# Kernel optimization log

Hardware: AMD Instinct MI355X
Metric: run time of the kernel (lower is better)

## Reference

```python
import jax, jax.numpy as jnp
import numpy as np

N = 50000          # nodes
E = 800000         # edges (avg degree 16)
F = 128            # in_dim = num_hidden*heads = pred_dim
H = 4              # attention heads per layer
D = 32             # num_hidden (per-head dim)
R = 11             # rel_num
L = 2              # num_layers
SCALE = float(1.0 / np.sqrt(D))


def setup_inputs() -> dict:
    key = jax.random.key(0)
    ks = jax.random.split(key, 16)
    inputs = jax.random.normal(ks[0], (N, F), jnp.float32)
    edge_types = jax.random.randint(ks[1], (E,), 0, R)
    src = jax.random.randint(ks[2], (E,), 0, N)
    dst = jax.random.randint(ks[3], (E,), 0, N)
    centrality = jax.random.uniform(ks[4], (N,), jnp.float32)
    rel_emb = jax.random.normal(ks[5], (R, F), jnp.float32) * 0.1
    # stacked per-layer projection weights (both layers have F -> H*D = F)
    Wq = jax.random.normal(ks[6], (L, F, H * D), jnp.float32) * 0.05
    Wk = jax.random.normal(ks[7], (L, F, H * D), jnp.float32) * 0.05
    Wv = jax.random.normal(ks[8], (L, F, H * D), jnp.float32) * 0.05
    We = jax.random.normal(ks[9], (L, F, H * D), jnp.float32) * 0.05
    bq = jnp.zeros((L, H * D), jnp.float32)
    bk = jnp.zeros((L, H * D), jnp.float32)
    bv = jnp.zeros((L, H * D), jnp.float32)
    be = jnp.zeros((L, H * D), jnp.float32)
    W_out = jax.random.normal(ks[10], (H * D, 1), jnp.float32) * 0.05
    b_out = jnp.zeros((1,), jnp.float32)
    gamma = jnp.ones((1,), jnp.float32)
    beta = jnp.zeros((1,), jnp.float32)
    return {"inputs": inputs, "edge_types": edge_types, "src": src, "dst": dst,
            "centrality": centrality, "rel_emb": rel_emb,
            "Wq": Wq, "bq": bq, "Wk": Wk, "bk": bk, "Wv": Wv, "bv": bv,
            "We": We, "be": be, "W_out": W_out, "b_out": b_out,
            "gamma": gamma, "beta": beta}


def _segment_softmax(score, dst, n):
    # score: [E, H]; softmax over incoming edges of each dst node
    m = jax.ops.segment_max(score, dst, num_segments=n)          # [N, H]
    ex = jnp.exp(score - m[dst])                                  # [E, H]
    s = jax.ops.segment_sum(ex, dst, num_segments=n)              # [N, H]
    return ex / (s[dst] + 1e-9)


def reference(inputs, edge_types, src, dst, centrality, rel_emb,
              Wq, bq, Wk, bk, Wv, bv, We, be, W_out, b_out, gamma, beta):
    h = inputs                                   # [N, F]
    ef = rel_emb[edge_types]                     # [E, pred_dim] relational edge embedding
    for l in range(L):
        q = (h @ Wq[l] + bq[l]).reshape(N, H, D)
        k = (h @ Wk[l] + bk[l]).reshape(N, H, D)
        v = (h @ Wv[l] + bv[l]).reshape(N, H, D)
        e = (ef @ We[l] + be[l]).reshape(E, H, D)
        # edge_mode="add": edge features added to keys/values on each edge
        ke = k[src] + e                           # [E, H, D]
        score = jnp.sum(q[dst] * ke, axis=-1) * SCALE   # [E, H]
        attn = _segment_softmax(score, dst, N)          # [E, H]
        msg = attn[:, :, None] * (v[src] + e)           # [E, H, D]
        agg = jax.ops.segment_sum(msg, dst, num_segments=N)  # [N, H, D]
        # identity residual (in_dim == H*D) + ELU activation
        h = jax.nn.elu(agg.reshape(N, H * D) + h)
    logits = h @ W_out + b_out                    # [N, 1]
    logits = jax.nn.relu((centrality * gamma + beta)[:, None] * logits)
    return logits
```

## Files before the change

kernel.cpp:

```cpp
#include <hip/hip_runtime.h>
#include <hip/hip_bf16.h>
#include <math.h>

#define SCALE_C 0.17677669529663687f
#define CAPP 64

typedef short bf16x8 __attribute__((ext_vector_type(8)));
typedef float f32x4 __attribute__((ext_vector_type(4)));


__global__ __launch_bounds__(256) void scatter_pad_k(
    const int* __restrict__ dst, const int* __restrict__ src, const int* __restrict__ etype,
    int E, int* __restrict__ cnt, int* __restrict__ bins) {
  int e = blockIdx.x * 256 + threadIdx.x;
  if (e < E) {
    int d = dst[e];
    int pos = atomicAdd(&cnt[d], 1);
    if (pos < CAPP) bins[(d << 6) + pos] = src[e] | (etype[e] << 20);
  }
}


__global__ __launch_bounds__(256) void prep_k(
    const float* __restrict__ Wq, const float* __restrict__ Wk, const float* __restrict__ Wv,
    __hip_bfloat16* __restrict__ wf,
    const float* __restrict__ rel_emb, const float* __restrict__ We, const float* __restrict__ be,
    float* __restrict__ re, int R, int* __restrict__ cnt, int N, int reb) {
  int b = blockIdx.x;
  if (b < 48) {
    int tid = b * 256 + threadIdx.x;
    int lane = tid & 63;
    int frag = tid >> 6;
    int ks = frag & 3;
    int ct = (frag >> 2) & 7;
    int mat = frag >> 5;
    int l = mat / 3, m = mat % 3;
    const float* W = ((m == 0) ? Wq : (m == 1) ? Wk : Wv) + (size_t)l * 128 * 128;
    int nn = ct * 16 + (lane & 15);
    int k0 = ks * 32 + (lane >> 4) * 8;
    __hip_bfloat16 tmp[8];
    #pragma unroll
    for (int j = 0; j < 8; ++j) tmp[j] = __float2bfloat16(W[(size_t)(k0 + j) * 128 + nn]);
    *(uint4*)&wf[(size_t)frag * 64 * 8 + (size_t)lane * 8] = *(const uint4*)tmp;
  } else if (b < 48 + reb) {
    int idx = (b - 48) * 256 + threadIdx.x;
    int tot = 2 * R * 128;
    if (idx >= tot) return;
    int c = idx & 127;
    int r = (idx >> 7) % R;
    int l = idx / (R * 128);
    const float* W = We + (size_t)l * 128 * 128;
    float acc = be[l * 128 + c];
    for (int kk = 0; kk < 128; ++kk) acc += rel_emb[r * 128 + kk] * W[kk * 128 + c];
    re[idx] = acc;
  } else {
    int idx = (b - 48 - reb) * 256 + threadIdx.x;
    int nq = N >> 2;
    if (idx < nq) ((uint4*)cnt)[idx] = make_uint4(0, 0, 0, 0);
    if (idx == nq) for (int k = nq << 2; k < N; ++k) cnt[k] = 0;
  }
}


__global__ __launch_bounds__(128) void qkv_k(
    const float* __restrict__ X, const __hip_bfloat16* __restrict__ wf,
    const float* __restrict__ bq, const float* __restrict__ bk, const float* __restrict__ bv,
    __hip_bfloat16* __restrict__ qo, __hip_bfloat16* __restrict__ kvo, int n) {
  __shared__ __hip_bfloat16 kvt[2][32][264];
  int wid = threadIdx.x >> 6;
  int lane = threadIdx.x & 63;
  int row0 = blockIdx.x * 64 + wid * 32;
  if (row0 >= n) return;
  int cl = lane & 15;
  int quad = lane >> 4;

  bf16x8 afrag[2][4];
  #pragma unroll
  for (int s = 0; s < 2; ++s) {
    int arow = row0 + s * 16 + cl;
    bool av = arow < n;
    const float* xr = X + (size_t)arow * 128 + quad * 8;
    #pragma unroll
    for (int ks = 0; ks < 4; ++ks) {
      float4 x0 = av ? *(const float4*)(xr + ks * 32)     : make_float4(0.f, 0.f, 0.f, 0.f);
      float4 x1 = av ? *(const float4*)(xr + ks * 32 + 4) : make_float4(0.f, 0.f, 0.f, 0.f);
      union { bf16x8 v; __hip_bfloat16 h[8]; } fu;
      fu.h[0] = __float2bfloat16(x0.x); fu.h[1] = __float2bfloat16(x0.y);
      fu.h[2] = __float2bfloat16(x0.z); fu.h[3] = __float2bfloat16(x0.w);
      fu.h[4] = __float2bfloat16(x1.x); fu.h[5] = __float2bfloat16(x1.y);
      fu.h[6] = __float2bfloat16(x1.z); fu.h[7] = __float2bfloat16(x1.w);
      afrag[s][ks] = fu.v;
    }
  }
  const uint4* wfu = (const uint4*)wf;

  #pragma unroll
  for (int ct = 0; ct < 8; ++ct) {
    f32x4 a0 = {0.f, 0.f, 0.f, 0.f}, a1 = {0.f, 0.f, 0.f, 0.f};
    #pragma unroll
    for (int ks = 0; ks < 4; ++ks) {
      uint4 braw = wfu[((size_t)ct * 4 + ks) * 64 + lane];
      bf16x8 bfr = __builtin_bit_cast(bf16x8, braw);
      a0 = __builtin_amdgcn_mfma_f32_16x16x32_bf16(afrag[0][ks], bfr, a0, 0, 0, 0);
      a1 = __builtin_amdgcn_mfma_f32_16x16x32_bf16(afrag[1][ks], bfr, a1, 0, 0, 0);
    }
    int c = ct * 16 + cl;
    float bb = bq[c];
    #pragma unroll
    for (int r = 0; r < 4; ++r) {
      kvt[wid][quad * 4 + r][c]      = __float2bfloat16((a0[r] + bb) * SCALE_C);
      kvt[wid][16 + quad * 4 + r][c] = __float2bfloat16((a1[r] + bb) * SCALE_C);
    }
  }
  {
    const uint4* tsrc = (const uint4*)&kvt[wid][0][0];
    #pragma unroll
    for (int it = 0; it < 8; ++it) {
      int idx = it * 64 + lane;
      int row = idx >> 4, g = idx & 15;
      if (row0 + row < n)
        *(uint4*)&qo[((size_t)(row0 + row)) * 128 + g * 8] = tsrc[row * 33 + g];
    }
  }

  #pragma unroll
  for (int m = 1; m <= 2; ++m) {
    const float* bias = (m == 1) ? bk : bv;
    #pragma unroll
    for (int ct = 0; ct < 8; ++ct) {
      f32x4 a0 = {0.f, 0.f, 0.f, 0.f}, a1 = {0.f, 0.f, 0.f, 0.f};
      #pragma unroll
      for (int ks = 0; ks < 4; ++ks) {
        uint4 braw = wfu[((size_t)(m * 8 + ct) * 4 + ks) * 64 + lane];
        bf16x8 bfr = __builtin_bit_cast(bf16x8, braw);
        a0 = __builtin_amdgcn_mfma_f32_16x16x32_bf16(afrag[0][ks], bfr, a0, 0, 0, 0);
        a1 = __builtin_amdgcn_mfma_f32_16x16x32_bf16(afrag[1][ks], bfr, a1, 0, 0, 0);
      }
      int c = ct * 16 + cl;
      float bb = bias[c];
      int p = 8 * (c >> 2) + (c & 3) + ((m == 2) ? 4 : 0);
      #pragma unroll
      for (int r = 0; r < 4; ++r) {
        kvt[wid][quad * 4 + r][p]      = __float2bfloat16(a0[r] + bb);
        kvt[wid][16 + quad * 4 + r][p] = __float2bfloat16(a1[r] + bb);
      }
    }
  }
  {
    const uint4* tsrc = (const uint4*)&kvt[wid][0][0];
    #pragma unroll
    for (int it = 0; it < 16; ++it) {
      int idx = it * 64 + lane;
      int row = idx >> 5, off = idx & 31;
      if (row0 + row < n)
        *(uint4*)&kvo[((size_t)(row0 + row)) * 256 + off * 8] = tsrc[row * 33 + off];
    }
  }
}


__global__ __launch_bounds__(256) void edge_k(
    const __hip_bfloat16* __restrict__ qb, const __hip_bfloat16* __restrict__ kv,
    const float* __restrict__ re,
    const int* __restrict__ bins, const int* __restrict__ cnt,
    const float* __restrict__ h_in, float* __restrict__ h_out,
    const float* __restrict__ Wout, const float* __restrict__ bout,
    const float* __restrict__ cent, const float* __restrict__ gamma,
    const float* __restrict__ beta, float* __restrict__ outp, int n) {
  int node = blockIdx.x * 4 + (threadIdx.x >> 6);
  if (node >= n) return;
  int lane = threadIdx.x & 63;
  int j = lane & 15;
  int quarter = lane >> 4;
  int rs = node << 6;
  int deg = cnt[node];
  deg = deg < CAPP ? deg : CAPP;

  uint4 qraw = *((const uint4*)(qb + ((size_t)node << 7)) + j);
  float qa0 = __uint_as_float(qraw.x << 16), qa1 = __uint_as_float(qraw.x & 0xffff0000u);
  float qa2 = __uint_as_float(qraw.y << 16), qa3 = __uint_as_float(qraw.y & 0xffff0000u);
  float qa4 = __uint_as_float(qraw.z << 16), qa5 = __uint_as_float(qraw.z & 0xffff0000u);
  float qa6 = __uint_as_float(qraw.w << 16), qa7 = __uint_as_float(qraw.w & 0xffff0000u);

  float ssum = 0.f;
  float acc0 = 0.f, acc1 = 0.f, acc2 = 0.f, acc3 = 0.f;
  float acc4 = 0.f, acc5 = 0.f, acc6 = 0.f, acc7 = 0.f;
  int nit = (deg + 3) >> 2;

  int pk1 = (quarter < deg) ? bins[rs + quarter] : 0;
  int pk2 = (quarter + 4 < deg) ? bins[rs + quarter + 4] : 0;
  uint s0 = (uint)pk1 & 0xFFFFFu, t0 = (uint)pk1 >> 20;
  const uint4* kr0 = (const uint4*)kv + (s0 * 32u + (uint)(j * 2));
  uint4 raw0 = kr0[0];
  uint4 raw1 = kr0[1];
  const float4* rr0 = (const float4*)re + (t0 * 32u + (uint)(j * 2));
  float4 r0 = rr0[0];
  float4 r1 = rr0[1];
  pk1 = pk2;

  for (int i = 0; i < nit; ++i) {
    int e2 = 4 * (i + 2) + quarter;
    pk2 = (e2 < deg) ? bins[rs + e2] : 0;
    uint s1 = (uint)pk1 & 0xFFFFFu, t1 = (uint)pk1 >> 20;
    const uint4* krn = (const uint4*)kv + (s1 * 32u + (uint)(j * 2));
    uint4 nraw0 = krn[0];
    uint4 nraw1 = krn[1];
    const float4* rrn = (const float4*)re + (t1 * 32u + (uint)(j * 2));
    float4 nr0 = rrn[0];
    float4 nr1 = rrn[1];

    bool valid = 4 * i + quarter < deg;
    float k0 = __uint_as_float(raw0.x << 16);
    float k1 = __uint_as_float(raw0.x & 0xffff0000u);
    float k2 = __uint_as_float(raw0.y << 16);
    float k3 = __uint_as_float(raw0.y & 0xffff0000u);
    float v0 = __uint_as_float(raw0.z << 16);
    float v1 = __uint_as_float(raw0.z & 0xffff0000u);
    float v2 = __uint_as_float(raw0.w << 16);
    float v3 = __uint_as_float(raw0.w & 0xffff0000u);
    float k4 = __uint_as_float(raw1.x << 16);
    float k5 = __uint_as_float(raw1.x & 0xffff0000u);
    float k6 = __uint_as_float(raw1.y << 16);
    float k7 = __uint_as_float(raw1.y & 0xffff0000u);
    float v4 = __uint_as_float(raw1.z << 16);
    float v5 = __uint_as_float(raw1.z & 0xffff0000u);
    float v6 = __uint_as_float(raw1.w << 16);
    float v7 = __uint_as_float(raw1.w & 0xffff0000u);
    float p = qa0 * (k0 + r0.x) + qa1 * (k1 + r0.y) + qa2 * (k2 + r0.z) + qa3 * (k3 + r0.w)
            + qa4 * (k4 + r1.x) + qa5 * (k5 + r1.y) + qa6 * (k6 + r1.z) + qa7 * (k7 + r1.w);
    p += __shfl_xor(p, 1);
    p += __shfl_xor(p, 2);
    float w = valid ? __expf(p) : 0.f;
    ssum += w;
    acc0 += w * (v0 + r0.x);
    acc1 += w * (v1 + r0.y);
    acc2 += w * (v2 + r0.z);
    acc3 += w * (v3 + r0.w);
    acc4 += w * (v4 + r1.x);
    acc5 += w * (v5 + r1.y);
    acc6 += w * (v6 + r1.z);
    acc7 += w * (v7 + r1.w);

    raw0 = nraw0; raw1 = nraw1; r0 = nr0; r1 = nr1;
    pk1 = pk2;
  }
  ssum += __shfl_xor(ssum, 16); ssum += __shfl_xor(ssum, 32);
  acc0 += __shfl_xor(acc0, 16); acc0 += __shfl_xor(acc0, 32);
  acc1 += __shfl_xor(acc1, 16); acc1 += __shfl_xor(acc1, 32);
  acc2 += __shfl_xor(acc2, 16); acc2 += __shfl_xor(acc2, 32);
  acc3 += __shfl_xor(acc3, 16); acc3 += __shfl_xor(acc3, 32);
  acc4 += __shfl_xor(acc4, 16); acc4 += __shfl_xor(acc4, 32);
  acc5 += __shfl_xor(acc5, 16); acc5 += __shfl_xor(acc5, 32);
  acc6 += __shfl_xor(acc6, 16); acc6 += __shfl_xor(acc6, 32);
  acc7 += __shfl_xor(acc7, 16); acc7 += __shfl_xor(acc7, 32);
  if (quarter != 0) return;

  float inv = 1.f / (ssum + 1e-9f);
  const float4* hrow = (const float4*)h_in + ((uint)node * 32u + (uint)(j * 2));
  float4 h0 = hrow[0], h1 = hrow[1];
  float x0 = acc0 * inv + h0.x;
  float x1 = acc1 * inv + h0.y;
  float x2 = acc2 * inv + h0.z;
  float x3 = acc3 * inv + h0.w;
  float x4 = acc4 * inv + h1.x;
  float x5 = acc5 * inv + h1.y;
  float x6 = acc6 * inv + h1.z;
  float x7 = acc7 * inv + h1.w;
  x0 = x0 > 0.f ? x0 : expm1f(x0);
  x1 = x1 > 0.f ? x1 : expm1f(x1);
  x2 = x2 > 0.f ? x2 : expm1f(x2);
  x3 = x3 > 0.f ? x3 : expm1f(x3);
  x4 = x4 > 0.f ? x4 : expm1f(x4);
  x5 = x5 > 0.f ? x5 : expm1f(x5);
  x6 = x6 > 0.f ? x6 : expm1f(x6);
  x7 = x7 > 0.f ? x7 : expm1f(x7);
  if (outp == nullptr) {
    float4* orow = (float4*)h_out + ((uint)node * 32u + (uint)(j * 2));
    orow[0] = make_float4(x0, x1, x2, x3);
    orow[1] = make_float4(x4, x5, x6, x7);
  } else {
    const float4* wrow = (const float4*)Wout + (uint)(j * 2);
    float4 w0 = wrow[0], w1 = wrow[1];
    float pp = x0 * w0.x + x1 * w0.y + x2 * w0.z + x3 * w0.w
             + x4 * w1.x + x5 * w1.y + x6 * w1.z + x7 * w1.w;
    pp += __shfl_xor(pp, 1);
    pp += __shfl_xor(pp, 2);
    pp += __shfl_xor(pp, 4);
    pp += __shfl_xor(pp, 8);
    if (lane == 0) {
      float lg = pp + bout[0];
      lg *= (cent[node] * gamma[0] + beta[0]);
      outp[node] = fmaxf(lg, 0.f);
    }
  }
}


extern "C" void kernel_launch(void* const* d_in, const int* in_sizes, int n_in,
                              void* d_out, int out_size, void* d_ws, size_t ws_size,
                              hipStream_t stream) {
  const float* inputs  = (const float*)d_in[0];
  const int*   etype   = (const int*)d_in[1];
  const int*   src     = (const int*)d_in[2];
  const int*   dst     = (const int*)d_in[3];
  const float* cent    = (const float*)d_in[4];
  const float* rel_emb = (const float*)d_in[5];
  const float* Wq      = (const float*)d_in[6];
  const float* bq      = (const float*)d_in[7];
  const float* Wk      = (const float*)d_in[8];
  const float* bk      = (const float*)d_in[9];
  const float* Wv      = (const float*)d_in[10];
  const float* bv      = (const float*)d_in[11];
  const float* We      = (const float*)d_in[12];
  const float* be      = (const float*)d_in[13];
  const float* Wout    = (const float*)d_in[14];
  const float* bout    = (const float*)d_in[15];
  const float* gamma   = (const float*)d_in[16];
  const float* beta    = (const float*)d_in[17];
  float* out = (float*)d_out;

  const int N = in_sizes[0] / 128;
  const int E = in_sizes[1];
  const int R = in_sizes[5] / 128;

  float* fw   = (float*)d_ws;
  float* hbuf = fw;
  float* re   = hbuf + (size_t)N * 128;
  __hip_bfloat16* qb = (__hip_bfloat16*)(re + 2 * (size_t)R * 128);
  __hip_bfloat16* kv = qb + (size_t)N * 128;
  __hip_bfloat16* wf = kv + (size_t)N * 256;
  int* cnt  = (int*)(wf + 6 * 16384);
  int* bins = cnt + N;

  int reb = (2 * R * 128 + 255) / 256;
  int zb  = (N / 4 + 256) / 256;
  prep_k<<<48 + reb + zb, 256, 0, stream>>>(Wq, Wk, Wv, wf, rel_emb, We, be, re, R, cnt, N, reb);
  int ebl = (E + 255) / 256;
  scatter_pad_k<<<ebl, 256, 0, stream>>>(dst, src, etype, E, cnt, bins);

  int qbks = (N + 63) / 64;
  int eb = (N + 3) / 4;
  for (int l = 0; l < 2; ++l) {
    const float* X = (l == 0) ? inputs : hbuf;
    size_t bo = (size_t)l * 128;
    qkv_k<<<qbks, 128, 0, stream>>>(X, wf + (size_t)l * 3 * 16384,
                                    bq + bo, bk + bo, bv + bo, qb, kv, N);
    edge_k<<<eb, 256, 0, stream>>>(qb, kv, re + (size_t)l * R * 128, bins, cnt,
                                   X, hbuf, Wout, bout, cent, gamma, beta,
                                   (l == 1) ? out : nullptr, N);
  }
}
```

Before: 310.0 us.

## Fuse edge binning with layer-0 QKV and store hidden state in bf16

The edge scatter/binning kernel and the layer-0 QKV projection are merged into one launch with disjoint block ranges so they can run concurrently. The cnt zeroing moves to hipMemsetAsync. The intermediate hidden state between layers is now stored in bf16 instead of fp32, so layer-1 QKV reads it without conversion and edge_k's residual read and write move half the bytes. The bf16 residual adds rounding error to the layer-1 input and residual path.

```diff
diff --git a/kernel.cpp b/kernel.cpp
--- a/kernel.cpp
+++ b/kernel.cpp
@@ -9,23 +9,11 @@
 typedef float f32x4 __attribute__((ext_vector_type(4)));
 
 
-__global__ __launch_bounds__(256) void scatter_pad_k(
-    const int* __restrict__ dst, const int* __restrict__ src, const int* __restrict__ etype,
-    int E, int* __restrict__ cnt, int* __restrict__ bins) {
-  int e = blockIdx.x * 256 + threadIdx.x;
-  if (e < E) {
-    int d = dst[e];
-    int pos = atomicAdd(&cnt[d], 1);
-    if (pos < CAPP) bins[(d << 6) + pos] = src[e] | (etype[e] << 20);
-  }
-}
-
-
-__global__ __launch_bounds__(256) void prep_k(
+__global__ __launch_bounds__(256) void prepA_k(
     const float* __restrict__ Wq, const float* __restrict__ Wk, const float* __restrict__ Wv,
     __hip_bfloat16* __restrict__ wf,
     const float* __restrict__ rel_emb, const float* __restrict__ We, const float* __restrict__ be,
-    float* __restrict__ re, int R, int* __restrict__ cnt, int N, int reb) {
+    float* __restrict__ re, int R) {
   int b = blockIdx.x;
   if (b < 48) {
     int tid = b * 256 + threadIdx.x;
@@ -42,7 +30,7 @@
     #pragma unroll
     for (int j = 0; j < 8; ++j) tmp[j] = __float2bfloat16(W[(size_t)(k0 + j) * 128 + nn]);
     *(uint4*)&wf[(size_t)frag * 64 * 8 + (size_t)lane * 8] = *(const uint4*)tmp;
-  } else if (b < 48 + reb) {
+  } else {
     int idx = (b - 48) * 256 + threadIdx.x;
     int tot = 2 * R * 128;
     if (idx >= tot) return;
@@ -51,25 +39,22 @@
     int l = idx / (R * 128);
     const float* W = We + (size_t)l * 128 * 128;
     float acc = be[l * 128 + c];
+    #pragma unroll 4
     for (int kk = 0; kk < 128; ++kk) acc += rel_emb[r * 128 + kk] * W[kk * 128 + c];
     re[idx] = acc;
-  } else {
-    int idx = (b - 48 - reb) * 256 + threadIdx.x;
-    int nq = N >> 2;
-    if (idx < nq) ((uint4*)cnt)[idx] = make_uint4(0, 0, 0, 0);
-    if (idx == nq) for (int k = nq << 2; k < N; ++k) cnt[k] = 0;
-  }
-}
-
-
-__global__ __launch_bounds__(128) void qkv_k(
-    const float* __restrict__ X, const __hip_bfloat16* __restrict__ wf,
+  }
+}
+
+
+__device__ __forceinline__ void qkv_body(
+    const float* __restrict__ Xf, const __hip_bfloat16* __restrict__ Xb,
+    const __hip_bfloat16* __restrict__ wf,
     const float* __restrict__ bq, const float* __restrict__ bk, const float* __restrict__ bv,
-    __hip_bfloat16* __restrict__ qo, __hip_bfloat16* __restrict__ kvo, int n) {
+    __hip_bfloat16* __restrict__ qo, __hip_bfloat16* __restrict__ kvo, int n, int bid) {
   __shared__ __hip_bfloat16 kvt[2][32][264];
   int wid = threadIdx.x >> 6;
   int lane = threadIdx.x & 63;
-  int row0 = blockIdx.x * 64 + wid * 32;
+  int row0 = bid * 64 + wid * 32;
   if (row0 >= n) return;
   int cl = lane & 15;
   int quad = lane >> 4;
@@ -79,17 +64,26 @@
   for (int s = 0; s < 2; ++s) {
     int arow = row0 + s * 16 + cl;
     bool av = arow < n;
-    const float* xr = X + (size_t)arow * 128 + quad * 8;
-    #pragma unroll
-    for (int ks = 0; ks < 4; ++ks) {
-      float4 x0 = av ? *(const float4*)(xr + ks * 32)     : make_float4(0.f, 0.f, 0.f, 0.f);
-      float4 x1 = av ? *(const float4*)(xr + ks * 32 + 4) : make_float4(0.f, 0.f, 0.f, 0.f);
-      union { bf16x8 v; __hip_bfloat16 h[8]; } fu;
-      fu.h[0] = __float2bfloat16(x0.x); fu.h[1] = __float2bfloat16(x0.y);
-      fu.h[2] = __float2bfloat16(x0.z); fu.h[3] = __float2bfloat16(x0.w);
-      fu.h[4] = __float2bfloat16(x1.x); fu.h[5] = __float2bfloat16(x1.y);
-      fu.h[6] = __float2bfloat16(x1.z); fu.h[7] = __float2bfloat16(x1.w);
-      afrag[s][ks] = fu.v;
+    if (Xb) {
+      const __hip_bfloat16* xr = Xb + (size_t)arow * 128 + quad * 8;
+      #pragma unroll
+      for (int ks = 0; ks < 4; ++ks) {
+        uint4 raw = av ? *(const uint4*)(xr + ks * 32) : make_uint4(0, 0, 0, 0);
+        afrag[s][ks] = __builtin_bit_cast(bf16x8, raw);
+      }
+    } else {
+      const float* xr = Xf + (size_t)arow * 128 + quad * 8;
+      #pragma unroll
+      for (int ks = 0; ks < 4; ++ks) {
+        float4 x0 = av ? *(const float4*)(xr + ks * 32)     : make_float4(0.f, 0.f, 0.f, 0.f);
+        float4 x1 = av ? *(const float4*)(xr + ks * 32 + 4) : make_float4(0.f, 0.f, 0.f, 0.f);
+        union { bf16x8 v; __hip_bfloat16 h[8]; } fu;
+        fu.h[0] = __float2bfloat16(x0.x); fu.h[1] = __float2bfloat16(x0.y);
+        fu.h[2] = __float2bfloat16(x0.z); fu.h[3] = __float2bfloat16(x0.w);
+        fu.h[4] = __float2bfloat16(x1.x); fu.h[5] = __float2bfloat16(x1.y);
+        fu.h[6] = __float2bfloat16(x1.z); fu.h[7] = __float2bfloat16(x1.w);
+        afrag[s][ks] = fu.v;
+      }
     }
   }
   const uint4* wfu = (const uint4*)wf;
@@ -159,11 +153,39 @@
 }
 
 
+__global__ __launch_bounds__(128) void megaB_k(
+    const int* __restrict__ dst, const int* __restrict__ src, const int* __restrict__ etype,
+    int E, int* __restrict__ cnt, int* __restrict__ bins,
+    const float* __restrict__ X, const __hip_bfloat16* __restrict__ wf,
+    const float* __restrict__ bq, const float* __restrict__ bk, const float* __restrict__ bv,
+    __hip_bfloat16* __restrict__ qo, __hip_bfloat16* __restrict__ kvo, int n, int SB) {
+  int b = blockIdx.x;
+  if (b < SB) {
+    int e = b * 128 + threadIdx.x;
+    if (e < E) {
+      int d = dst[e];
+      int pos = atomicAdd(&cnt[d], 1);
+      if (pos < CAPP) bins[(d << 6) + pos] = src[e] | (etype[e] << 20);
+    }
+  } else {
+    qkv_body(X, nullptr, wf, bq, bk, bv, qo, kvo, n, b - SB);
+  }
+}
+
+__global__ __launch_bounds__(128) void qkv2_k(
+    const __hip_bfloat16* __restrict__ Xb, const __hip_bfloat16* __restrict__ wf,
+    const float* __restrict__ bq, const float* __restrict__ bk, const float* __restrict__ bv,
+    __hip_bfloat16* __restrict__ qo, __hip_bfloat16* __restrict__ kvo, int n) {
+  qkv_body(nullptr, Xb, wf, bq, bk, bv, qo, kvo, n, blockIdx.x);
+}
+
+
 __global__ __launch_bounds__(256) void edge_k(
     const __hip_bfloat16* __restrict__ qb, const __hip_bfloat16* __restrict__ kv,
     const float* __restrict__ re,
     const int* __restrict__ bins, const int* __restrict__ cnt,
-    const float* __restrict__ h_in, float* __restrict__ h_out,
+    const float* __restrict__ h_in_f, const __hip_bfloat16* __restrict__ h_in_b,
+    __hip_bfloat16* __restrict__ h_out_b,
     const float* __restrict__ Wout, const float* __restrict__ bout,
     const float* __restrict__ cent, const float* __restrict__ gamma,
     const float* __restrict__ beta, float* __restrict__ outp, int n) {
@@ -256,8 +278,17 @@
   if (quarter != 0) return;
 
   float inv = 1.f / (ssum + 1e-9f);
-  const float4* hrow = (const float4*)h_in + ((uint)node * 32u + (uint)(j * 2));
-  float4 h0 = hrow[0], h1 = hrow[1];
+  float4 h0, h1;
+  if (h_in_b) {
+    uint4 hraw = *((const uint4*)(h_in_b + ((size_t)node << 7)) + j);
+    h0.x = __uint_as_float(hraw.x << 16); h0.y = __uint_as_float(hraw.x & 0xffff0000u);
+    h0.z = __uint_as_float(hraw.y << 16); h0.w = __uint_as_float(hraw.y & 0xffff0000u);
+    h1.x = __uint_as_float(hraw.z << 16); h1.y = __uint_as_float(hraw.z & 0xffff0000u);
+    h1.z = __uint_as_float(hraw.w << 16); h1.w = __uint_as_float(hraw.w & 0xffff0000u);
+  } else {
+    const float4* hrow = (const float4*)h_in_f + ((uint)node * 32u + (uint)(j * 2));
+    h0 = hrow[0]; h1 = hrow[1];
+  }
   float x0 = acc0 * inv + h0.x;
   float x1 = acc1 * inv + h0.y;
   float x2 = acc2 * inv + h0.z;
@@ -275,9 +306,12 @@
   x6 = x6 > 0.f ? x6 : expm1f(x6);
   x7 = x7 > 0.f ? x7 : expm1f(x7);
   if (outp == nullptr) {
-    float4* orow = (float4*)h_out + ((uint)node * 32u + (uint)(j * 2));
-    orow[0] = make_float4(x0, x1, x2, x3);
-    orow[1] = make_float4(x4, x5, x6, x7);
+    union { uint4 u; __hip_bfloat16 hh[8]; } P;
+    P.hh[0] = __float2bfloat16(x0); P.hh[1] = __float2bfloat16(x1);
+    P.hh[2] = __float2bfloat16(x2); P.hh[3] = __float2bfloat16(x3);
+    P.hh[4] = __float2bfloat16(x4); P.hh[5] = __float2bfloat16(x5);
+    P.hh[6] = __float2bfloat16(x6); P.hh[7] = __float2bfloat16(x7);
+    *((uint4*)(h_out_b + ((size_t)node << 7)) + j) = P.u;
   } else {
     const float4* wrow = (const float4*)Wout + (uint)(j * 2);
     float4 w0 = wrow[0], w1 = wrow[1];
@@ -323,30 +357,31 @@
   const int E = in_sizes[1];
   const int R = in_sizes[5] / 128;
 
-  float* fw   = (float*)d_ws;
-  float* hbuf = fw;
-  float* re   = hbuf + (size_t)N * 128;
-  __hip_bfloat16* qb = (__hip_bfloat16*)(re + 2 * (size_t)R * 128);
+  float* re = (float*)d_ws;
+  __hip_bfloat16* hb = (__hip_bfloat16*)(re + 2 * (size_t)R * 128);
+  __hip_bfloat16* qb = hb + (size_t)N * 128;
   __hip_bfloat16* kv = qb + (size_t)N * 128;
   __hip_bfloat16* wf = kv + (size_t)N * 256;
   int* cnt  = (int*)(wf + 6 * 16384);
   int* bins = cnt + N;
 
+  hipMemsetAsync(cnt, 0, (size_t)N * sizeof(int), stream);
+
   int reb = (2 * R * 128 + 255) / 256;
-  int zb  = (N / 4 + 256) / 256;
-  prep_k<<<48 + reb + zb, 256, 0, stream>>>(Wq, Wk, Wv, wf, rel_emb, We, be, re, R, cnt, N, reb);
-  int ebl = (E + 255) / 256;
-  scatter_pad_k<<<ebl, 256, 0, stream>>>(dst, src, etype, E, cnt, bins);
-
-  int qbks = (N + 63) / 64;
+  prepA_k<<<48 + reb, 256, 0, stream>>>(Wq, Wk, Wv, wf, rel_emb, We, be, re, R);
+
+  int SB = (E + 127) / 128;
+  int QB = (N + 63) / 64;
+  megaB_k<<<SB + QB, 128, 0, stream>>>(dst, src, etype, E, cnt, bins,
+                                       inputs, wf, bq, bk, bv, qb, kv, N, SB);
+
   int eb = (N + 3) / 4;
-  for (int l = 0; l < 2; ++l) {
-    const float* X = (l == 0) ? inputs : hbuf;
-    size_t bo = (size_t)l * 128;
-    qkv_k<<<qbks, 128, 0, stream>>>(X, wf + (size_t)l * 3 * 16384,
-                                    bq + bo, bk + bo, bv + bo, qb, kv, N);
-    edge_k<<<eb, 256, 0, stream>>>(qb, kv, re + (size_t)l * R * 128, bins, cnt,
-                                   X, hbuf, Wout, bout, cent, gamma, beta,
-                                   (l == 1) ? out : nullptr, N);
-  }
-}
+  edge_k<<<eb, 256, 0, stream>>>(qb, kv, re, bins, cnt,
+                                 inputs, nullptr, hb,
+                                 Wout, bout, cent, gamma, beta, nullptr, N);
+  qkv2_k<<<QB, 128, 0, stream>>>(hb, wf + (size_t)3 * 16384,
+                                 bq + 128, bk + 128, bv + 128, qb, kv, N);
+  edge_k<<<eb, 256, 0, stream>>>(qb, kv, re + (size_t)R * 128, bins, cnt,
+                                 nullptr, hb, nullptr,
+                                 Wout, bout, cent, gamma, beta, out, N);
+}
```

Result: no change. 314.5 us (+1.4%).
